# Optimization experiments

Measured on AMD Instinct MI355X. Metric: run time of the kernel, lower is better.

## Reference

```python
import jax, jax.numpy as jnp
import numpy as np
import math

D_MODEL = 1024
NUM_HEADS = 16
N_GROUP = 4
HEAD_DIM = D_MODEL // NUM_HEADS  # 64
KV_DIM = N_GROUP * HEAD_DIM      # 256
BS, SEQ = 2, 2048


def setup_inputs() -> dict:
    key = jax.random.key(0)
    ks = jax.random.split(key, 7)
    s = 0.02
    return {
        "h": jax.random.normal(ks[0], (BS, SEQ, D_MODEL), dtype=jnp.float32),
        "wq_w": jax.random.normal(ks[1], (D_MODEL, D_MODEL), dtype=jnp.float32) * s,
        "wq_b": jnp.zeros((D_MODEL,), dtype=jnp.float32),
        "wk_w": jax.random.normal(ks[2], (KV_DIM, D_MODEL), dtype=jnp.float32) * s,
        "wk_b": jnp.zeros((KV_DIM,), dtype=jnp.float32),
        "wv_w": jax.random.normal(ks[3], (KV_DIM, D_MODEL), dtype=jnp.float32) * s,
        "wv_b": jnp.zeros((KV_DIM,), dtype=jnp.float32),
    }


def reference(h, wq_w, wq_b, wk_w, wk_b, wv_w, wv_b):
    bs, seq, _ = h.shape
    rep = NUM_HEADS // N_GROUP  # heads per KV group

    # Linear projections (torch Linear: x @ W.T + b)
    q = h @ wq_w.T + wq_b                     # [bs, seq, d_model]
    k = h @ wk_w.T + wk_b                     # [bs, seq, kv_dim]
    v = h @ wv_w.T + wv_b                     # [bs, seq, kv_dim]

    q = q.reshape(bs, seq, NUM_HEADS, HEAD_DIM).transpose(0, 2, 1, 3)  # [b,H,s,d]
    k = k.reshape(bs, seq, N_GROUP, HEAD_DIM)                          # [b,s,G,d]
    v = v.reshape(bs, seq, N_GROUP, HEAD_DIM)
    # torch .repeat(1,1,1,rep).view(...,num_heads,head_dim) maps head h -> group h//rep,
    # identical to repeating each group `rep` times consecutively along the head axis.
    k = jnp.repeat(k, rep, axis=2).transpose(0, 2, 1, 3)               # [b,H,s,d]
    v = jnp.repeat(v, rep, axis=2).transpose(0, 2, 1, 3)               # [b,H,s,d]

    scores = jnp.einsum("bhqd,bhkd->bhqk", q, k) / math.sqrt(HEAD_DIM)
    attn = jax.nn.softmax(scores, axis=-1)
    out = jnp.einsum("bhqk,bhkd->bhqd", attn, v)                       # [b,H,s,d]
    out = out.transpose(0, 2, 1, 3).reshape(bs, seq, NUM_HEADS * HEAD_DIM)
    return out
```

## Files before the change

kernel.cpp:

```cpp
#include <hip/hip_runtime.h>

typedef _Float16 f16;
typedef _Float16 f16x8 __attribute__((ext_vector_type(8)));
typedef _Float16 f16x4 __attribute__((ext_vector_type(4)));
typedef float f32x4 __attribute__((ext_vector_type(4)));

#define MFMA16(a, b, c) __builtin_amdgcn_mfma_f32_16x16x32_f16((a), (b), (c), 0, 0, 0)
#define GLDS16(g, l)                                                        \
    __builtin_amdgcn_global_load_lds(                                       \
        (const __attribute__((address_space(1))) void*)(g),                 \
        (__attribute__((address_space(3))) void*)(l), 16, 0, 0)

#define SEQ 2048
#define DMODEL 1024
#define NH 16
#define NG 4
#define PAD 76

__global__ __launch_bounds__(256) void cvt_all(const float* __restrict__ h,
                                               const float* __restrict__ wq,
                                               const float* __restrict__ wk,
                                               const float* __restrict__ wv,
                                               f16* __restrict__ hb, f16* __restrict__ wqb,
                                               f16* __restrict__ wkb, f16* __restrict__ wvb) {
    const int i = blockIdx.x * 256 + threadIdx.x;
    const float* s; f16* d; int off;
    if (i < 1048576)      { s = h;  d = hb;  off = i; }
    else if (i < 1310720) { s = wq; d = wqb; off = i - 1048576; }
    else if (i < 1376256) { s = wk; d = wkb; off = i - 1310720; }
    else                  { s = wv; d = wvb; off = i - 1376256; }
    const float4 v = ((const float4*)s)[off];
    f16x4 p;
    p[0] = (f16)v.x; p[1] = (f16)v.y; p[2] = (f16)v.z; p[3] = (f16)v.w;
    ((f16x4*)d)[off] = p;
}

__global__ __launch_bounds__(256, 3) void qkv_gemm(const f16* __restrict__ hA,
                                                   const f16* __restrict__ wq,
                                                   const f16* __restrict__ wk,
                                                   const f16* __restrict__ wv,
                                                   const float* __restrict__ bq,
                                                   const float* __restrict__ bk,
                                                   const float* __restrict__ bv,
                                                   f16* __restrict__ Qb,
                                                   f16* __restrict__ Kb,
                                                   f16* __restrict__ Vtb,
                                                   float qscale) {
    __shared__ __align__(16) f16 As[128 * 32];
    __shared__ __align__(16) f16 Bs[64 * 32];

    const int tid  = threadIdx.x;
    const int lane = tid & 63;
    const int l15  = lane & 15;
    const int l4   = lane >> 4;
    const int wave = tid >> 6;
    const int wm   = (wave >> 1) * 64;
    const int wn   = (wave & 1) * 32;
    const int bx   = blockIdx.x;
    const int m0   = blockIdx.y * 128;

    const f16* W; const float* bias; f16* C; int N, n0; float osc; int vmode;
    if (bx < 16)      { W = wq; bias = bq; C = Qb;  N = 1024; n0 = bx * 64;        osc = qscale; vmode = 0; }
    else if (bx < 20) { W = wk; bias = bk; C = Kb;  N = 256;  n0 = (bx - 16) * 64; osc = 1.0f;   vmode = 0; }
    else              { W = wv; bias = bv; C = Vtb; N = 256;  n0 = (bx - 20) * 64; osc = 1.0f;   vmode = 1; }

    const int rowT = tid >> 2;
    const int colT = (tid & 3) * 8;
    const f16* Ag = hA + (size_t)(m0 + rowT) * DMODEL + colT;
    const f16* Bg = W  + (size_t)(n0 + rowT) * DMODEL + colT;
    f16* AsW0 = As + wave * 512;
    f16* AsW1 = As + 2048 + wave * 512;
    f16* BsW  = Bs + wave * 512;

    f32x4 acc[4][2];
#pragma unroll
    for (int i = 0; i < 4; i++)
#pragma unroll
        for (int j = 0; j < 2; j++) acc[i][j] = (f32x4)0.0f;

    for (int k0 = 0; k0 < DMODEL; k0 += 32) {
        GLDS16(Ag + k0,         AsW0);
        GLDS16(Ag + 65536 + k0, AsW1);
        GLDS16(Bg + k0,         BsW);
        __syncthreads();

        f16x8 af[4], bf[2];
#pragma unroll
        for (int i = 0; i < 4; i++)
            af[i] = *(const f16x8*)&As[(wm + i * 16 + l15) * 32 + l4 * 8];
#pragma unroll
        for (int j = 0; j < 2; j++)
            bf[j] = *(const f16x8*)&Bs[(wn + j * 16 + l15) * 32 + l4 * 8];
#pragma unroll
        for (int i = 0; i < 4; i++)
#pragma unroll
            for (int j = 0; j < 2; j++)
                acc[i][j] = MFMA16(af[i], bf[j], acc[i][j]);
        __syncthreads();
    }

#pragma unroll
    for (int i = 0; i < 4; i++) {
        const int mbase = m0 + wm + i * 16 + l4 * 4;
#pragma unroll
        for (int j = 0; j < 2; j++) {
            const int n  = n0 + wn + j * 16 + l15;
            const float bv = bias[n];
            if (vmode == 0) {
#pragma unroll
                for (int r = 0; r < 4; r++)
                    C[(size_t)(mbase + r) * N + n] = (f16)((acc[i][j][r] + bv) * osc);
            } else {
                f16x4 p;
#pragma unroll
                for (int r = 0; r < 4; r++)
                    p[r] = (f16)((acc[i][j][r] + bv) * osc);
                const int bb = mbase >> 11;
                const int s  = mbase & 2047;
                *(f16x4*)&C[((size_t)(bb * 256 + n)) * SEQ + s] = p;
            }
        }
    }
}

__global__ __launch_bounds__(256, 2) void attn_kernel(const f16* __restrict__ Q,
                                                      const f16* __restrict__ Kt,
                                                      const f16* __restrict__ Vt,
                                                      float* __restrict__ out) {
    __shared__ __align__(16) f16 Ks[64 * PAD];
    __shared__ __align__(16) f16 Vs[64 * PAD];
    __shared__ __align__(16) f16 Ps[128 * PAD];

    const int tid  = threadIdx.x;
    const int lane = tid & 63;
    const int l15  = lane & 15;
    const int l4   = lane >> 4;
    const int wave = tid >> 6;
    const int b    = blockIdx.z;
    const int hp   = blockIdx.y;
    const int g    = hp >> 1;
    const int q0   = blockIdx.x * 64;
    const int qw   = wave * 16;

    f16x8 qf[2][2];
#pragma unroll
    for (int h = 0; h < 2; h++)
#pragma unroll
        for (int kt = 0; kt < 2; kt++)
            qf[h][kt] = *(const f16x8*)&Q[((size_t)(b * SEQ + q0 + qw + l15)) * DMODEL
                                          + (hp * 2 + h) * 64 + kt * 32 + l4 * 8];

    f32x4 oacc[2][4];
    float lsum[2][4];
#pragma unroll
    for (int h = 0; h < 2; h++)
#pragma unroll
        for (int dt = 0; dt < 4; dt++) oacc[h][dt] = (f32x4)0.0f;
#pragma unroll
    for (int h = 0; h < 2; h++)
#pragma unroll
        for (int r = 0; r < 4; r++) lsum[h][r] = 0.0f;

    const int srow = tid >> 2;
    const int sc8  = (tid & 3) * 8;
    const f16* Kg = Kt + (size_t)(b * SEQ + srow) * 256 + g * 64 + sc8;
    const f16* Vg = Vt + (size_t)(b * 256 + g * 64 + srow) * SEQ + sc8;

    for (int kb = 0; kb < SEQ; kb += 64) {
        *(f16x8*)&Ks[srow * PAD + sc8]      = *(const f16x8*)(Kg + (size_t)kb * 256);
        *(f16x8*)&Ks[srow * PAD + 32 + sc8] = *(const f16x8*)(Kg + (size_t)kb * 256 + 32);
        *(f16x8*)&Vs[srow * PAD + sc8]      = *(const f16x8*)(Vg + kb);
        *(f16x8*)&Vs[srow * PAD + 32 + sc8] = *(const f16x8*)(Vg + kb + 32);
        __syncthreads();

        f32x4 sacc[2][4];
#pragma unroll
        for (int h = 0; h < 2; h++)
#pragma unroll
            for (int jt = 0; jt < 4; jt++) sacc[h][jt] = (f32x4)0.0f;
#pragma unroll
        for (int jt = 0; jt < 4; jt++) {
            const f16x8 kf0 = *(const f16x8*)&Ks[(jt * 16 + l15) * PAD + l4 * 8];
            const f16x8 kf1 = *(const f16x8*)&Ks[(jt * 16 + l15) * PAD + 32 + l4 * 8];
#pragma unroll
            for (int h = 0; h < 2; h++) {
                sacc[h][jt] = MFMA16(qf[h][0], kf0, sacc[h][jt]);
                sacc[h][jt] = MFMA16(qf[h][1], kf1, sacc[h][jt]);
            }
        }

#pragma unroll
        for (int h = 0; h < 2; h++)
#pragma unroll
            for (int jt = 0; jt < 4; jt++)
#pragma unroll
                for (int r = 0; r < 4; r++) {
                    const float p = exp2f(fminf(sacc[h][jt][r], 14.0f));
                    lsum[h][r] += p;
                    Ps[(h * 64 + qw + l4 * 4 + r) * PAD + jt * 16 + l15] = (f16)p;
                }

#pragma unroll
        for (int kt = 0; kt < 2; kt++) {
            const f16x8 pf0 = *(const f16x8*)&Ps[(qw + l15) * PAD + kt * 32 + l4 * 8];
            const f16x8 pf1 = *(const f16x8*)&Ps[(64 + qw + l15) * PAD + kt * 32 + l4 * 8];
#pragma unroll
            for (int dt = 0; dt < 4; dt++) {
                const f16x8 vf = *(const f16x8*)&Vs[(dt * 16 + l15) * PAD + kt * 32 + l4 * 8];
                oacc[0][dt] = MFMA16(pf0, vf, oacc[0][dt]);
                oacc[1][dt] = MFMA16(pf1, vf, oacc[1][dt]);
            }
        }
        __syncthreads();
    }

#pragma unroll
    for (int h = 0; h < 2; h++)
#pragma unroll
        for (int r = 0; r < 4; r++) {
            float l = lsum[h][r];
            l += __shfl_xor(l, 1);
            l += __shfl_xor(l, 2);
            l += __shfl_xor(l, 4);
            l += __shfl_xor(l, 8);
            const float inv = 1.0f / l;
            const int q = q0 + qw + l4 * 4 + r;
            float* op = out + ((size_t)(b * SEQ + q)) * DMODEL + (hp * 2 + h) * 64;
#pragma unroll
            for (int dt = 0; dt < 4; dt++)
                op[dt * 16 + l15] = oacc[h][dt][r] * inv;
        }
}

extern "C" void kernel_launch(void* const* d_in, const int* in_sizes, int n_in,
                              void* d_out, int out_size, void* d_ws, size_t ws_size,
                              hipStream_t stream) {
    const float* h    = (const float*)d_in[0];
    const float* wq_w = (const float*)d_in[1];
    const float* wq_b = (const float*)d_in[2];
    const float* wk_w = (const float*)d_in[3];
    const float* wk_b = (const float*)d_in[4];
    const float* wv_w = (const float*)d_in[5];
    const float* wv_b = (const float*)d_in[6];
    float* out = (float*)d_out;

    char* ws = (char*)d_ws;
    f16* hb  = (f16*)(ws + 0);
    f16* wqb = (f16*)(ws + 8388608);
    f16* wkb = (f16*)(ws + 10485760);
    f16* wvb = (f16*)(ws + 11010048);
    f16* Qb  = (f16*)(ws + 11534336);
    f16* Kb  = (f16*)(ws + 19922944);
    f16* Vtb = (f16*)(ws + 22020096);

    cvt_all<<<5632, 256, 0, stream>>>(h, wq_w, wk_w, wv_w, hb, wqb, wkb, wvb);

    const float qscale = 0.125f * 1.4426950408889634f;
    qkv_gemm<<<dim3(24, 32), 256, 0, stream>>>(hb, wqb, wkb, wvb, wq_b, wk_b, wv_b,
                                               Qb, Kb, Vtb, qscale);

    attn_kernel<<<dim3(32, 8, 2), 256, 0, stream>>>(Qb, Kb, Vtb, out);
}
```

Before: 191.6 us.

## Retile QKV GEMM to 512-thread 128x128 blocks and use one head per attention block

The QKV projection GEMM now uses 512-thread blocks computing 128x128 output tiles, which halves the grid and shares each A tile across more columns. The attention kernel now gives each block one head instead of two. That doubles the grid, halves the Ps buffer and register use, and allows 4 blocks per CU. The trade-off is that each K/V tile loaded into LDS is reused by only one head, so K/V global traffic doubles, while occupancy and wave-level parallelism go up.

```diff
diff --git a/kernel.cpp b/kernel.cpp
--- a/kernel.cpp
+++ b/kernel.cpp
@@ -35,42 +35,40 @@
     ((f16x4*)d)[off] = p;
 }
 
-__global__ __launch_bounds__(256, 3) void qkv_gemm(const f16* __restrict__ hA,
-                                                   const f16* __restrict__ wq,
-                                                   const f16* __restrict__ wk,
-                                                   const f16* __restrict__ wv,
-                                                   const float* __restrict__ bq,
-                                                   const float* __restrict__ bk,
-                                                   const float* __restrict__ bv,
-                                                   f16* __restrict__ Qb,
-                                                   f16* __restrict__ Kb,
-                                                   f16* __restrict__ Vtb,
-                                                   float qscale) {
+__global__ __launch_bounds__(512) void qkv_gemm(const f16* __restrict__ hA,
+                                                const f16* __restrict__ wq,
+                                                const f16* __restrict__ wk,
+                                                const f16* __restrict__ wv,
+                                                const float* __restrict__ bq,
+                                                const float* __restrict__ bk,
+                                                const float* __restrict__ bv,
+                                                f16* __restrict__ Qb,
+                                                f16* __restrict__ Kb,
+                                                f16* __restrict__ Vtb,
+                                                float qscale) {
     __shared__ __align__(16) f16 As[128 * 32];
-    __shared__ __align__(16) f16 Bs[64 * 32];
+    __shared__ __align__(16) f16 Bs[128 * 32];
 
     const int tid  = threadIdx.x;
     const int lane = tid & 63;
     const int l15  = lane & 15;
     const int l4   = lane >> 4;
     const int wave = tid >> 6;
-    const int wm   = (wave >> 1) * 64;
-    const int wn   = (wave & 1) * 32;
+    const int wm   = (wave & 1) * 64;
+    const int wn   = (wave >> 1) * 32;
     const int bx   = blockIdx.x;
     const int m0   = blockIdx.y * 128;
 
     const f16* W; const float* bias; f16* C; int N, n0; float osc; int vmode;
-    if (bx < 16)      { W = wq; bias = bq; C = Qb;  N = 1024; n0 = bx * 64;        osc = qscale; vmode = 0; }
-    else if (bx < 20) { W = wk; bias = bk; C = Kb;  N = 256;  n0 = (bx - 16) * 64; osc = 1.0f;   vmode = 0; }
-    else              { W = wv; bias = bv; C = Vtb; N = 256;  n0 = (bx - 20) * 64; osc = 1.0f;   vmode = 1; }
+    if (bx < 8)       { W = wq; bias = bq; C = Qb;  N = 1024; n0 = bx * 128;        osc = qscale; vmode = 0; }
+    else if (bx < 10) { W = wk; bias = bk; C = Kb;  N = 256;  n0 = (bx - 8) * 128;  osc = 1.0f;   vmode = 0; }
+    else              { W = wv; bias = bv; C = Vtb; N = 256;  n0 = (bx - 10) * 128; osc = 1.0f;   vmode = 1; }
 
     const int rowT = tid >> 2;
     const int colT = (tid & 3) * 8;
     const f16* Ag = hA + (size_t)(m0 + rowT) * DMODEL + colT;
     const f16* Bg = W  + (size_t)(n0 + rowT) * DMODEL + colT;
-    f16* AsW0 = As + wave * 512;
-    f16* AsW1 = As + 2048 + wave * 512;
-    f16* BsW  = Bs + wave * 512;
+    const int sOff = wave * 512;
 
     f32x4 acc[4][2];
 #pragma unroll
@@ -79,9 +77,8 @@
         for (int j = 0; j < 2; j++) acc[i][j] = (f32x4)0.0f;
 
     for (int k0 = 0; k0 < DMODEL; k0 += 32) {
-        GLDS16(Ag + k0,         AsW0);
-        GLDS16(Ag + 65536 + k0, AsW1);
-        GLDS16(Bg + k0,         BsW);
+        GLDS16(Ag + k0, As + sOff);
+        GLDS16(Bg + k0, Bs + sOff);
         __syncthreads();
 
         f16x8 af[4], bf[2];
@@ -123,13 +120,13 @@
     }
 }
 
-__global__ __launch_bounds__(256, 2) void attn_kernel(const f16* __restrict__ Q,
+__global__ __launch_bounds__(256, 4) void attn_kernel(const f16* __restrict__ Q,
                                                       const f16* __restrict__ Kt,
                                                       const f16* __restrict__ Vt,
                                                       float* __restrict__ out) {
     __shared__ __align__(16) f16 Ks[64 * PAD];
     __shared__ __align__(16) f16 Vs[64 * PAD];
-    __shared__ __align__(16) f16 Ps[128 * PAD];
+    __shared__ __align__(16) f16 Ps[64 * PAD];
 
     const int tid  = threadIdx.x;
     const int lane = tid & 63;
@@ -137,29 +134,22 @@
     const int l4   = lane >> 4;
     const int wave = tid >> 6;
     const int b    = blockIdx.z;
-    const int hp   = blockIdx.y;
-    const int g    = hp >> 1;
+    const int hh   = blockIdx.y;
+    const int g    = hh >> 2;
     const int q0   = blockIdx.x * 64;
     const int qw   = wave * 16;
 
-    f16x8 qf[2][2];
-#pragma unroll
-    for (int h = 0; h < 2; h++)
-#pragma unroll
-        for (int kt = 0; kt < 2; kt++)
-            qf[h][kt] = *(const f16x8*)&Q[((size_t)(b * SEQ + q0 + qw + l15)) * DMODEL
-                                          + (hp * 2 + h) * 64 + kt * 32 + l4 * 8];
-
-    f32x4 oacc[2][4];
-    float lsum[2][4];
-#pragma unroll
-    for (int h = 0; h < 2; h++)
-#pragma unroll
-        for (int dt = 0; dt < 4; dt++) oacc[h][dt] = (f32x4)0.0f;
-#pragma unroll
-    for (int h = 0; h < 2; h++)
-#pragma unroll
-        for (int r = 0; r < 4; r++) lsum[h][r] = 0.0f;
+    f16x8 qf[2];
+#pragma unroll
+    for (int kt = 0; kt < 2; kt++)
+        qf[kt] = *(const f16x8*)&Q[((size_t)(b * SEQ + q0 + qw + l15)) * DMODEL + hh * 64 + kt * 32 + l4 * 8];
+
+    f32x4 oacc[4];
+    float lsum[4];
+#pragma unroll
+    for (int dt = 0; dt < 4; dt++) oacc[dt] = (f32x4)0.0f;
+#pragma unroll
+    for (int r = 0; r < 4; r++) lsum[r] = 0.0f;
 
     const int srow = tid >> 2;
     const int sc8  = (tid & 3) * 8;
@@ -173,63 +163,52 @@
         *(f16x8*)&Vs[srow * PAD + 32 + sc8] = *(const f16x8*)(Vg + kb + 32);
         __syncthreads();
 
-        f32x4 sacc[2][4];
-#pragma unroll
-        for (int h = 0; h < 2; h++)
-#pragma unroll
-            for (int jt = 0; jt < 4; jt++) sacc[h][jt] = (f32x4)0.0f;
+        f32x4 sacc[4];
+#pragma unroll
+        for (int jt = 0; jt < 4; jt++) sacc[jt] = (f32x4)0.0f;
 #pragma unroll
         for (int jt = 0; jt < 4; jt++) {
             const f16x8 kf0 = *(const f16x8*)&Ks[(jt * 16 + l15) * PAD + l4 * 8];
             const f16x8 kf1 = *(const f16x8*)&Ks[(jt * 16 + l15) * PAD + 32 + l4 * 8];
-#pragma unroll
-            for (int h = 0; h < 2; h++) {
-                sacc[h][jt] = MFMA16(qf[h][0], kf0, sacc[h][jt]);
-                sacc[h][jt] = MFMA16(qf[h][1], kf1, sacc[h][jt]);
+            sacc[jt] = MFMA16(qf[0], kf0, sacc[jt]);
+            sacc[jt] = MFMA16(qf[1], kf1, sacc[jt]);
+        }
+
+#pragma unroll
+        for (int jt = 0; jt < 4; jt++)
+#pragma unroll
+            for (int r = 0; r < 4; r++) {
+                const float p = exp2f(fminf(sacc[jt][r], 14.0f));
+                lsum[r] += p;
+                Ps[(qw + l4 * 4 + r) * PAD + jt * 16 + l15] = (f16)p;
+            }
+
+#pragma unroll
+        for (int kt = 0; kt < 2; kt++) {
+            const f16x8 pf = *(const f16x8*)&Ps[(qw + l15) * PAD + kt * 32 + l4 * 8];
+#pragma unroll
+            for (int dt = 0; dt < 4; dt++) {
+                const f16x8 vf = *(const f16x8*)&Vs[(dt * 16 + l15) * PAD + kt * 32 + l4 * 8];
+                oacc[dt] = MFMA16(pf, vf, oacc[dt]);
             }
         }
-
-#pragma unroll
-        for (int h = 0; h < 2; h++)
-#pragma unroll
-            for (int jt = 0; jt < 4; jt++)
-#pragma unroll
-                for (int r = 0; r < 4; r++) {
-                    const float p = exp2f(fminf(sacc[h][jt][r], 14.0f));
-                    lsum[h][r] += p;
-                    Ps[(h * 64 + qw + l4 * 4 + r) * PAD + jt * 16 + l15] = (f16)p;
-                }
-
-#pragma unroll
-        for (int kt = 0; kt < 2; kt++) {
-            const f16x8 pf0 = *(const f16x8*)&Ps[(qw + l15) * PAD + kt * 32 + l4 * 8];
-            const f16x8 pf1 = *(const f16x8*)&Ps[(64 + qw + l15) * PAD + kt * 32 + l4 * 8];
-#pragma unroll
-            for (int dt = 0; dt < 4; dt++) {
-                const f16x8 vf = *(const f16x8*)&Vs[(dt * 16 + l15) * PAD + kt * 32 + l4 * 8];
-                oacc[0][dt] = MFMA16(pf0, vf, oacc[0][dt]);
-                oacc[1][dt] = MFMA16(pf1, vf, oacc[1][dt]);
-            }
-        }
-        __syncthreads();
-    }
-
-#pragma unroll
-    for (int h = 0; h < 2; h++)
-#pragma unroll
-        for (int r = 0; r < 4; r++) {
-            float l = lsum[h][r];
-            l += __shfl_xor(l, 1);
-            l += __shfl_xor(l, 2);
-            l += __shfl_xor(l, 4);
-            l += __shfl_xor(l, 8);
-            const float inv = 1.0f / l;
-            const int q = q0 + qw + l4 * 4 + r;
-            float* op = out + ((size_t)(b * SEQ + q)) * DMODEL + (hp * 2 + h) * 64;
-#pragma unroll
-            for (int dt = 0; dt < 4; dt++)
-                op[dt * 16 + l15] = oacc[h][dt][r] * inv;
-        }
+        __syncthreads();
+    }
+
+#pragma unroll
+    for (int r = 0; r < 4; r++) {
+        float l = lsum[r];
+        l += __shfl_xor(l, 1);
+        l += __shfl_xor(l, 2);
+        l += __shfl_xor(l, 4);
+        l += __shfl_xor(l, 8);
+        const float inv = 1.0f / l;
+        const int q = q0 + qw + l4 * 4 + r;
+        float* op = out + ((size_t)(b * SEQ + q)) * DMODEL + hh * 64;
+#pragma unroll
+        for (int dt = 0; dt < 4; dt++)
+            op[dt * 16 + l15] = oacc[dt][r] * inv;
+    }
 }
 
 extern "C" void kernel_launch(void* const* d_in, const int* in_sizes, int n_in,
@@ -256,8 +235,8 @@
     cvt_all<<<5632, 256, 0, stream>>>(h, wq_w, wk_w, wv_w, hb, wqb, wkb, wvb);
 
     const float qscale = 0.125f * 1.4426950408889634f;
-    qkv_gemm<<<dim3(24, 32), 256, 0, stream>>>(hb, wqb, wkb, wvb, wq_b, wk_b, wv_b,
+    qkv_gemm<<<dim3(12, 32), 512, 0, stream>>>(hb, wqb, wkb, wvb, wq_b, wk_b, wv_b,
                                                Qb, Kb, Vtb, qscale);
 
-    attn_kernel<<<dim3(32, 8, 2), 256, 0, stream>>>(Qb, Kb, Vtb, out);
-}
+    attn_kernel<<<dim3(32, 16, 2), 256, 0, stream>>>(Qb, Kb, Vtb, out);
+}
```

Result: no change. 190.5 us (-0.6%).
